# Performance work log

Measured on AMD Instinct MI355X. Metric: run time of the kernel, lower is better.

## Reference

```python
import jax, jax.numpy as jnp
import numpy as np

IN_F = 4096
OUT_F = 4096
NNZ = 167772  # int(IN_F*OUT_F*0.01)
B, S = 4, 2048
ALPHA = 1.0  # self.alpha (privacy enabled)


def setup_inputs() -> dict:
    key = jax.random.key(0)
    k1, k2, k3, k4, k5 = jax.random.split(key, 5)
    x = jax.random.normal(k1, (B, S, IN_F), dtype=jnp.float32)
    # quantized-then-dequantized base weights stored in fp16
    base_weights = (jax.random.normal(k2, (OUT_F, IN_F), dtype=jnp.float32) * 0.02).astype(jnp.float16)
    # sparse outlier residual in COO form (equivalent to the module's CSR buffers)
    ortho_rows = jax.random.randint(k3, (NNZ,), 0, OUT_F, dtype=jnp.int32)
    ortho_cols = jax.random.randint(k4, (NNZ,), 0, IN_F, dtype=jnp.int32)
    ortho_vals = (jax.random.normal(k5, (NNZ,), dtype=jnp.float32) * 1e-3).astype(jnp.float16)
    return {"x": x, "base_weights": base_weights, "ortho_vals": ortho_vals,
            "ortho_rows": ortho_rows, "ortho_cols": ortho_cols}


def reference(x, base_weights, ortho_vals, ortho_rows, ortho_cols):
    orig_shape = x.shape
    orig_dtype = x.dtype
    x_flat = x.reshape(-1, IN_F)                                   # [N, in]
    # Base stream: fp16 GEMM, accumulated to fp32 (matches torch.mm on fp16 then .to(f32))
    out_base = jnp.matmul(x_flat.astype(jnp.float16), base_weights.T).astype(jnp.float32)  # [N, out]
    # Ortho stream: sparse CSR residual, computed in fp32 (vals upcast like the module)
    # Scatter the nnz outliers into a dense [out, in] matrix once, then a single GEMM
    # (same math as torch.sparse.mm over the CSR tensor, without per-chunk loops).
    w_ortho = jnp.zeros((OUT_F, IN_F), jnp.float32).at[ortho_rows, ortho_cols].add(
        ortho_vals.astype(jnp.float32))
    out_ortho = jnp.matmul(x_flat.astype(jnp.float32), w_ortho.T)  # [N, out]
    out_flat = out_base + ALPHA * out_ortho
    return out_flat.reshape(orig_shape[:-1] + (OUT_F,)).astype(orig_dtype)
```

## Files before the change

kernel.cpp:

```cpp
#include <hip/hip_runtime.h>
#include <stdint.h>

#define IN_F 4096
#define OUT_F 4096
#define NTOK 8192
#define NNZ_CNT 167772

typedef __attribute__((ext_vector_type(4))) float f32x4;
typedef __attribute__((ext_vector_type(8))) __bf16 bf16x8;
typedef __attribute__((ext_vector_type(8))) unsigned short u16x8;

__device__ __forceinline__ unsigned short f2bf(float f) {
  union { float f; unsigned int i; } u; u.f = f;
  unsigned int i = u.i;
  unsigned int r = (i + 0x7FFFu + ((i >> 16) & 1u)) >> 16;
  return (unsigned short)r;
}
__device__ __forceinline__ float bf2f(unsigned short h) {
  union { unsigned int i; float f; } u; u.i = ((unsigned int)h) << 16;
  return u.f;
}
__device__ __forceinline__ float sanitize(float f, float lim) {
  if (f >= -lim && f <= lim) return f;
  if (f > lim) return lim;
  if (f < -lim) return -lim;
  return 0.f;
}

__device__ __forceinline__ bool detect_isf32(const unsigned short* w, int tid, int* sh_cnt) {
  if (tid == 0) *sh_cnt = 0;
  __syncthreads();
  int local = 0;
  if (tid < 256) {
    for (int j = 0; j < 16; ++j) {
      unsigned short u = w[tid * 16 + j];
      int e = (u >> 7) & 0xFF;
      if (u != 0 && e >= 107 && e <= 126) local++;
    }
  }
  atomicAdd(sh_cnt, local);
  __syncthreads();
  return *sh_cnt < 3481;
}

__global__ void prep_kernel(const float4* __restrict__ x, u16x8* __restrict__ xb, int n8x,
                            const void* __restrict__ bw, u16x8* __restrict__ wc, int n8w) {
  __shared__ int sh_cnt;
  const bool isf32 = detect_isf32((const unsigned short*)bw, threadIdx.x, &sh_cnt);
  const int stride = gridDim.x * blockDim.x;
  const int i0 = blockIdx.x * blockDim.x + threadIdx.x;
  for (int i = i0; i < n8x; i += stride) {
    float4 v0 = x[i * 2], v1 = x[i * 2 + 1];
    u16x8 o;
    o[0] = f2bf(sanitize(v0.x, 64.f)); o[1] = f2bf(sanitize(v0.y, 64.f));
    o[2] = f2bf(sanitize(v0.z, 64.f)); o[3] = f2bf(sanitize(v0.w, 64.f));
    o[4] = f2bf(sanitize(v1.x, 64.f)); o[5] = f2bf(sanitize(v1.y, 64.f));
    o[6] = f2bf(sanitize(v1.z, 64.f)); o[7] = f2bf(sanitize(v1.w, 64.f));
    xb[i] = o;
  }
  for (int i = i0; i < n8w; i += stride) {
    u16x8 o;
    if (isf32) {
      const float4* s = (const float4*)bw + i * 2;
      float4 v0 = s[0], v1 = s[1];
      o[0] = f2bf(sanitize(v0.x, 1.f)); o[1] = f2bf(sanitize(v0.y, 1.f));
      o[2] = f2bf(sanitize(v0.z, 1.f)); o[3] = f2bf(sanitize(v0.w, 1.f));
      o[4] = f2bf(sanitize(v1.x, 1.f)); o[5] = f2bf(sanitize(v1.y, 1.f));
      o[6] = f2bf(sanitize(v1.z, 1.f)); o[7] = f2bf(sanitize(v1.w, 1.f));
    } else {
      u16x8 v = ((const u16x8*)bw)[i];
#pragma unroll
      for (int j = 0; j < 8; ++j) o[j] = f2bf(sanitize(bf2f(v[j]), 1.f));
    }
    wc[i] = o;
  }
}

__global__ void scatter_kernel(const void* __restrict__ vals,
                               const int* __restrict__ rows,
                               const int* __restrict__ cols,
                               unsigned short* __restrict__ W,
                               const void* __restrict__ bw_probe) {
  __shared__ int sh_cnt;
  const bool isf32 = detect_isf32((const unsigned short*)bw_probe, threadIdx.x, &sh_cnt);
  int i = blockIdx.x * blockDim.x + threadIdx.x;
  if (i >= NNZ_CNT) return;
  int r = rows[i], c = cols[i];
  if ((unsigned)r >= OUT_F || (unsigned)c >= IN_F) return;
  float v = isf32 ? ((const float*)vals)[i] : bf2f(((const unsigned short*)vals)[i]);
  v = sanitize(v, 1.f);
  unsigned int* addr = (unsigned int*)(W + (size_t)r * IN_F + (c & ~1));
  bool hi = (c & 1);
  unsigned int old = *addr, assumed;
  do {
    assumed = old;
    unsigned short h = hi ? (unsigned short)(assumed >> 16) : (unsigned short)(assumed & 0xFFFFu);
    unsigned short nh = f2bf(bf2f(h) + v);
    unsigned int nw = hi ? ((assumed & 0x0000FFFFu) | ((unsigned int)nh << 16))
                         : ((assumed & 0xFFFF0000u) | (unsigned int)nh);
    old = atomicCAS(addr, assumed, nw);
  } while (old != assumed);
}

#define GLOAD16(g, l)                                                                  \
  __builtin_amdgcn_global_load_lds((const __attribute__((address_space(1))) void*)(g), \
                                   (__attribute__((address_space(3))) void*)(l), 16, 0, 0)

__global__ __launch_bounds__(512, 2) void gemm256_kernel(
    const unsigned short* __restrict__ Abf,
    const unsigned short* __restrict__ Bw,
    float* __restrict__ C) {
  __shared__ __align__(16) char lds[131072];
  const int t = threadIdx.x;
  const int l = t & 63;
  const int wv = t >> 6;
  const int wm = wv >> 2;
  const int wn = wv & 3;
  const int l15 = l & 15;

  const int swz = (blockIdx.x & 7) * 64 + (blockIdx.x >> 3);
  const int bm = (swz >> 4) * 256;
  const int bn = (swz & 15) * 256;

  const int srow = t >> 2;
  const int sunit = (t & 3) ^ ((t >> 3) & 3);
  const unsigned short* aS0 = Abf + (size_t)(bm + srow) * IN_F + sunit * 8;
  const unsigned short* aS1 = aS0 + (size_t)128 * IN_F;
  const unsigned short* bS0 = Bw + (size_t)(bn + srow) * IN_F + sunit * 8;
  const unsigned short* bS1 = bS0 + (size_t)128 * IN_F;
  char* dstA = (char*)lds + wv * 1024;
  char* dstB = (char*)lds + 32768 + wv * 1024;

  const int u = (l >> 4) ^ ((l15 >> 1) & 3);
  const int iA = (wm * 128 + l15) * 4 + u;
  const int iB = 2048 + (wn * 64 + l15) * 4 + u;
  const bf16x8* smp = (const bf16x8*)lds;

  f32x4 acc[8][4] = {};

  GLOAD16(aS0 + 0, dstA + 0);          GLOAD16(aS1 + 0, dstA + 8192);
  GLOAD16(bS0 + 0, dstB + 0);          GLOAD16(bS1 + 0, dstB + 8192);
  GLOAD16(aS0 + 32, dstA + 16384);     GLOAD16(aS1 + 32, dstA + 16384 + 8192);
  GLOAD16(bS0 + 32, dstB + 16384);     GLOAD16(bS1 + 32, dstB + 16384 + 8192);
  GLOAD16(aS0 + 64, dstA + 65536);     GLOAD16(aS1 + 64, dstA + 65536 + 8192);
  GLOAD16(bS0 + 64, dstB + 65536);     GLOAD16(bS1 + 64, dstB + 65536 + 8192);

  for (int kt = 0; kt < 64; ++kt) {
    const int c = kt & 1;
    const int cU = c << 12;
    const int s1 = ((kt + 1 < 64) ? (kt + 1) : 63) * 64 + 32;
    const int s2 = ((kt + 2 < 64) ? (kt + 2) : 63) * 64;
    const int d1 = (c ^ 1) * 65536 + 16384;
    const int d2 = c * 65536;
    bf16x8 av[4], bv[4], av1[8], bv1[4];

    asm volatile("s_waitcnt vmcnt(4)" ::: "memory");
    asm volatile("s_barrier" ::: "memory");

#pragma unroll
    for (int mi = 0; mi < 4; ++mi) av[mi] = smp[cU + iA + mi * 64];
#pragma unroll
    for (int ni = 0; ni < 4; ++ni) bv[ni] = smp[cU + iB + ni * 64];
    GLOAD16(aS0 + s1, dstA + d1);
    GLOAD16(aS1 + s1, dstA + d1 + 8192);
    __builtin_amdgcn_s_setprio(1);
#pragma unroll
    for (int mi = 0; mi < 4; ++mi)
#pragma unroll
      for (int ni = 0; ni < 4; ++ni)
        acc[mi][ni] = __builtin_amdgcn_mfma_f32_16x16x32_bf16(av[mi], bv[ni], acc[mi][ni], 0, 0, 0);
    __builtin_amdgcn_s_setprio(0);

#pragma unroll
    for (int mi = 0; mi < 4; ++mi) av[mi] = smp[cU + iA + (mi + 4) * 64];
    GLOAD16(bS0 + s1, dstB + d1);
    GLOAD16(bS1 + s1, dstB + d1 + 8192);
    __builtin_amdgcn_s_setprio(1);
#pragma unroll
    for (int mi = 0; mi < 4; ++mi)
#pragma unroll
      for (int ni = 0; ni < 4; ++ni)
        acc[mi + 4][ni] = __builtin_amdgcn_mfma_f32_16x16x32_bf16(av[mi], bv[ni], acc[mi + 4][ni], 0, 0, 0);
    __builtin_amdgcn_s_setprio(0);

#pragma unroll
    for (int mi = 0; mi < 8; ++mi) av1[mi] = smp[cU + 1024 + iA + mi * 64];
#pragma unroll
    for (int ni = 0; ni < 4; ++ni) bv1[ni] = smp[cU + 1024 + iB + ni * 64];

    asm volatile("s_barrier" ::: "memory");
    asm volatile("s_waitcnt lgkmcnt(0)" ::: "memory");

    GLOAD16(aS0 + s2, dstA + d2);
    GLOAD16(aS1 + s2, dstA + d2 + 8192);
    __builtin_amdgcn_s_setprio(1);
#pragma unroll
    for (int mi = 0; mi < 4; ++mi)
#pragma unroll
      for (int ni = 0; ni < 4; ++ni)
        acc[mi][ni] = __builtin_amdgcn_mfma_f32_16x16x32_bf16(av1[mi], bv1[ni], acc[mi][ni], 0, 0, 0);
    __builtin_amdgcn_s_setprio(0);

    GLOAD16(bS0 + s2, dstB + d2);
    GLOAD16(bS1 + s2, dstB + d2 + 8192);
    __builtin_amdgcn_s_setprio(1);
#pragma unroll
    for (int mi = 0; mi < 4; ++mi)
#pragma unroll
      for (int ni = 0; ni < 4; ++ni)
        acc[mi + 4][ni] = __builtin_amdgcn_mfma_f32_16x16x32_bf16(av1[mi + 4], bv1[ni], acc[mi + 4][ni], 0, 0, 0);
    __builtin_amdgcn_s_setprio(0);
  }

#pragma unroll
  for (int mi = 0; mi < 8; ++mi) {
#pragma unroll
    for (int ni = 0; ni < 4; ++ni) {
      int row0 = bm + wm * 128 + mi * 16 + ((l >> 4) << 2);
      int col = bn + wn * 64 + ni * 16 + l15;
#pragma unroll
      for (int r = 0; r < 4; ++r)
        C[(size_t)(row0 + r) * OUT_F + col] = acc[mi][ni][r];
    }
  }
}

__global__ __launch_bounds__(256, 3) void gemm_kernel(
    const float* __restrict__ Af, const unsigned short* __restrict__ Bw, float* __restrict__ C) {
  __shared__ bf16x8 smem[2048];
  const int tid = threadIdx.x;
  const int lane = tid & 63;
  const int wv = tid >> 6;
  const int bm = blockIdx.x * 128;
  const int bn = blockIdx.y * 128;
  const int srow = wv * 8 + (lane >> 3);
  const int scol = (lane & 7) * 8;
  const int wr = wv >> 1, wc = wv & 1;
  f32x4 acc[4][4] = {};
  const float* afp[4];
  const unsigned short* bptr[4];
#pragma unroll
  for (int q = 0; q < 4; ++q) {
    afp[q] = Af + (size_t)(bm + q * 32 + srow) * IN_F + scol;
    bptr[q] = Bw + (size_t)(bn + q * 32 + srow) * IN_F + scol;
  }
  char* smbase = (char*)smem;
  for (int k0 = 0; k0 < IN_F; k0 += 64) {
    __syncthreads();
#pragma unroll
    for (int q = 0; q < 4; ++q)
      GLOAD16(bptr[q] + k0, smbase + 16384 + q * 4096 + wv * 1024);
#pragma unroll
    for (int q = 0; q < 4; ++q) {
      const float* s = afp[q] + k0;
      float4 v0 = ((const float4*)s)[0];
      float4 v1 = ((const float4*)s)[1];
      u16x8 p;
      p[0] = f2bf(sanitize(v0.x, 64.f)); p[1] = f2bf(sanitize(v0.y, 64.f));
      p[2] = f2bf(sanitize(v0.z, 64.f)); p[3] = f2bf(sanitize(v0.w, 64.f));
      p[4] = f2bf(sanitize(v1.x, 64.f)); p[5] = f2bf(sanitize(v1.y, 64.f));
      p[6] = f2bf(sanitize(v1.z, 64.f)); p[7] = f2bf(sanitize(v1.w, 64.f));
      ((u16x8*)smem)[q * 256 + wv * 64 + lane] = p;
    }
    __syncthreads();
#pragma unroll
    for (int kk = 0; kk < 2; ++kk) {
      bf16x8 av[4], bv[4];
#pragma unroll
      for (int m = 0; m < 4; ++m)
        av[m] = smem[(wr * 64 + m * 16 + (lane & 15)) * 8 + kk * 4 + (lane >> 4)];
#pragma unroll
      for (int n = 0; n < 4; ++n)
        bv[n] = smem[1024 + (wc * 64 + n * 16 + (lane & 15)) * 8 + kk * 4 + (lane >> 4)];
#pragma unroll
      for (int m = 0; m < 4; ++m)
#pragma unroll
        for (int n = 0; n < 4; ++n)
          acc[m][n] = __builtin_amdgcn_mfma_f32_16x16x32_bf16(av[m], bv[n], acc[m][n], 0, 0, 0);
    }
  }
#pragma unroll
  for (int m = 0; m < 4; ++m)
#pragma unroll
    for (int n = 0; n < 4; ++n) {
      int row0 = bm + wr * 64 + m * 16 + ((lane >> 4) << 2);
      int col = bn + wc * 64 + n * 16 + (lane & 15);
#pragma unroll
      for (int r = 0; r < 4; ++r)
        C[(size_t)(row0 + r) * OUT_F + col] = acc[m][n][r];
    }
}

__global__ void naive_gemm_kernel(const float* __restrict__ x, const void* __restrict__ W,
                                  float* __restrict__ out) {
  __shared__ int sh_cnt;
  const bool isf32 = detect_isf32((const unsigned short*)W, threadIdx.x, &sh_cnt);
  int o = blockIdx.x * 256 + threadIdx.x;
  int t = blockIdx.y;
  const float* xr = x + (size_t)t * IN_F;
  float acc = 0.f;
  if (isf32) {
    const float* wr = (const float*)W + (size_t)o * IN_F;
    for (int k = 0; k < IN_F; ++k) acc += bf2f(f2bf(xr[k])) * bf2f(f2bf(sanitize(wr[k], 1.f)));
  } else {
    const unsigned short* wr = (const unsigned short*)W + (size_t)o * IN_F;
    for (int k = 0; k < IN_F; ++k) acc += bf2f(f2bf(xr[k])) * sanitize(bf2f(wr[k]), 1.f);
  }
  out[(size_t)t * OUT_F + o] = acc;
}
__global__ void naive_sparse_kernel(const float* __restrict__ x, const void* __restrict__ vals,
                                    const int* __restrict__ rows, const int* __restrict__ cols,
                                    float* __restrict__ out, const void* __restrict__ bw_probe) {
  __shared__ int sh_cnt;
  const bool isf32 = detect_isf32((const unsigned short*)bw_probe, threadIdx.x, &sh_cnt);
  int t = blockIdx.x * 256 + threadIdx.x;
  if (t >= NTOK) return;
  const float* xr = x + (size_t)t * IN_F;
  float* orow = out + (size_t)t * OUT_F;
  for (int i = 0; i < NNZ_CNT; ++i) {
    int r = rows[i], c = cols[i];
    if ((unsigned)r >= OUT_F || (unsigned)c >= IN_F) continue;
    float v = isf32 ? ((const float*)vals)[i] : bf2f(((const unsigned short*)vals)[i]);
    orow[r] += sanitize(v, 1.f) * xr[c];
  }
}

extern "C" void kernel_launch(void* const* d_in, const int* in_sizes, int n_in,
                              void* d_out, int out_size, void* d_ws, size_t ws_size,
                              hipStream_t stream) {
  (void)out_size;
  const int NX = NTOK * IN_F, NW = OUT_F * IN_F;
  int ix = -1, ib = -1, qs[3], nq = 0;
  for (int i = 0; i < n_in; ++i) {
    if (in_sizes[i] == NX) ix = i;
    else if (in_sizes[i] == NW) ib = i;
    else if (in_sizes[i] == NNZ_CNT && nq < 3) qs[nq++] = i;
  }
  if (ix < 0 || ib < 0 || nq < 3) { ix = 0; ib = 1; qs[0] = 2; qs[1] = 3; qs[2] = 4; }
  const float* x = (const float*)d_in[ix];
  const void* bw = d_in[ib];
  const int* rows = (const int*)d_in[qs[1]];
  const void* vals;
  const int* cols;
  if (ix < ib) { vals = d_in[qs[0]]; cols = (const int*)d_in[qs[2]]; }
  else         { vals = d_in[qs[2]]; cols = (const int*)d_in[qs[0]]; }
  float* out = (float*)d_out;

  const size_t w_bytes = (size_t)OUT_F * IN_F * 2;
  const size_t xb_bytes = (size_t)NTOK * IN_F * 2;

  if (ws_size < w_bytes + 64) {
    hipLaunchKernelGGL(naive_gemm_kernel, dim3(OUT_F / 256, NTOK), dim3(256), 0, stream,
                       x, bw, out);
    hipLaunchKernelGGL(naive_sparse_kernel, dim3((NTOK + 255) / 256), dim3(256), 0, stream,
                       x, vals, rows, cols, out, bw);
    return;
  }

  unsigned short* wcmb = (unsigned short*)d_ws;
  const bool big = ws_size >= w_bytes + xb_bytes;
  unsigned short* xb = (unsigned short*)((char*)d_ws + w_bytes);

  hipLaunchKernelGGL(prep_kernel, dim3(2048), dim3(256), 0, stream,
                     (const float4*)x, (u16x8*)xb, big ? (NX / 8) : 0,
                     bw, (u16x8*)wcmb, NW / 8);
  hipLaunchKernelGGL(scatter_kernel, dim3((NNZ_CNT + 255) / 256), dim3(256), 0, stream,
                     vals, rows, cols, wcmb, bw);

  if (big) {
    hipLaunchKernelGGL(gemm256_kernel, dim3((NTOK / 256) * (OUT_F / 256)), dim3(512), 0, stream,
                       xb, wcmb, out);
  } else {
    hipLaunchKernelGGL(gemm_kernel, dim3(NTOK / 128, OUT_F / 128), dim3(256), 0, stream,
                       x, wcmb, out);
  }
}
```

Measured before the change: 306.4 us.

## Shrink GEMM tile to 256x128 with triple-buffered K=32 stages

Reshapes the main bf16 GEMM block tile from 256x256 to 256x128. The 8 waves now form a 4x2 grid, each holding 64x64 accumulators instead of 128x64. The K loop changes from a double-buffered 64-wide step with split halves to a three-stage ring of 32-wide K slices, and LDS drops from 128KB to 72KB. The intent is to raise occupancy (launch bounds 4) and block count, for better latency hiding and load balance. The cost is less operand reuse per tile, more global/L2 traffic for the activations, and a barrier every 32 K instead of every 64.

```diff
diff --git a/kernel.cpp b/kernel.cpp
--- a/kernel.cpp
+++ b/kernel.cpp
@@ -106,63 +106,61 @@
   __builtin_amdgcn_global_load_lds((const __attribute__((address_space(1))) void*)(g), \
                                    (__attribute__((address_space(3))) void*)(l), 16, 0, 0)
 
-__global__ __launch_bounds__(512, 2) void gemm256_kernel(
+__global__ __launch_bounds__(512, 4) void gemm256_kernel(
     const unsigned short* __restrict__ Abf,
     const unsigned short* __restrict__ Bw,
     float* __restrict__ C) {
-  __shared__ __align__(16) char lds[131072];
+  __shared__ __align__(16) char lds[73728];
   const int t = threadIdx.x;
   const int l = t & 63;
   const int wv = t >> 6;
-  const int wm = wv >> 2;
-  const int wn = wv & 3;
+  const int wm = wv >> 1;
+  const int wn = wv & 1;
   const int l15 = l & 15;
 
-  const int swz = (blockIdx.x & 7) * 64 + (blockIdx.x >> 3);
-  const int bm = (swz >> 4) * 256;
-  const int bn = (swz & 15) * 256;
+  const int swz = (blockIdx.x & 7) * 128 + (blockIdx.x >> 3);
+  const int bm = (swz >> 5) * 256;
+  const int bn = (swz & 31) * 128;
 
   const int srow = t >> 2;
   const int sunit = (t & 3) ^ ((t >> 3) & 3);
   const unsigned short* aS0 = Abf + (size_t)(bm + srow) * IN_F + sunit * 8;
   const unsigned short* aS1 = aS0 + (size_t)128 * IN_F;
   const unsigned short* bS0 = Bw + (size_t)(bn + srow) * IN_F + sunit * 8;
-  const unsigned short* bS1 = bS0 + (size_t)128 * IN_F;
   char* dstA = (char*)lds + wv * 1024;
-  char* dstB = (char*)lds + 32768 + wv * 1024;
+  char* dstB = (char*)lds + 16384 + wv * 1024;
 
   const int u = (l >> 4) ^ ((l15 >> 1) & 3);
-  const int iA = (wm * 128 + l15) * 4 + u;
-  const int iB = 2048 + (wn * 64 + l15) * 4 + u;
+  const int iA = (wm * 64 + l15) * 4 + u;
+  const int iB = 1024 + (wn * 64 + l15) * 4 + u;
   const bf16x8* smp = (const bf16x8*)lds;
 
-  f32x4 acc[8][4] = {};
-
-  GLOAD16(aS0 + 0, dstA + 0);          GLOAD16(aS1 + 0, dstA + 8192);
-  GLOAD16(bS0 + 0, dstB + 0);          GLOAD16(bS1 + 0, dstB + 8192);
-  GLOAD16(aS0 + 32, dstA + 16384);     GLOAD16(aS1 + 32, dstA + 16384 + 8192);
-  GLOAD16(bS0 + 32, dstB + 16384);     GLOAD16(bS1 + 32, dstB + 16384 + 8192);
-  GLOAD16(aS0 + 64, dstA + 65536);     GLOAD16(aS1 + 64, dstA + 65536 + 8192);
-  GLOAD16(bS0 + 64, dstB + 65536);     GLOAD16(bS1 + 64, dstB + 65536 + 8192);
-
-  for (int kt = 0; kt < 64; ++kt) {
-    const int c = kt & 1;
-    const int cU = c << 12;
-    const int s1 = ((kt + 1 < 64) ? (kt + 1) : 63) * 64 + 32;
-    const int s2 = ((kt + 2 < 64) ? (kt + 2) : 63) * 64;
-    const int d1 = (c ^ 1) * 65536 + 16384;
-    const int d2 = c * 65536;
-    bf16x8 av[4], bv[4], av1[8], bv1[4];
-
-    asm volatile("s_waitcnt vmcnt(4)" ::: "memory");
+  f32x4 acc[4][4] = {};
+
+  GLOAD16(aS0 + 0, dstA + 0);
+  GLOAD16(aS1 + 0, dstA + 8192);
+  GLOAD16(bS0 + 0, dstB + 0);
+  GLOAD16(aS0 + 32, dstA + 24576);
+  GLOAD16(aS1 + 32, dstA + 24576 + 8192);
+  GLOAD16(bS0 + 32, dstB + 24576);
+
+  int c = 0;
+  for (int kt = 0; kt < 128; ++kt) {
+    const int c2 = (c >= 1) ? c - 1 : 2;
+    const int cU = c * 1536;
+    const int dA2 = c2 * 24576;
+    const int s2 = ((kt + 2 < 128) ? (kt + 2) : 127) * 32;
+    bf16x8 av[4], bv[4];
+
+    asm volatile("s_waitcnt vmcnt(3)" ::: "memory");
     asm volatile("s_barrier" ::: "memory");
-
 #pragma unroll
     for (int mi = 0; mi < 4; ++mi) av[mi] = smp[cU + iA + mi * 64];
+    GLOAD16(aS0 + s2, dstA + dA2);
+    GLOAD16(aS1 + s2, dstA + dA2 + 8192);
 #pragma unroll
     for (int ni = 0; ni < 4; ++ni) bv[ni] = smp[cU + iB + ni * 64];
-    GLOAD16(aS0 + s1, dstA + d1);
-    GLOAD16(aS1 + s1, dstA + d1 + 8192);
+    GLOAD16(bS0 + s2, dstB + dA2);
     __builtin_amdgcn_s_setprio(1);
 #pragma unroll
     for (int mi = 0; mi < 4; ++mi)
@@ -171,52 +169,14 @@
         acc[mi][ni] = __builtin_amdgcn_mfma_f32_16x16x32_bf16(av[mi], bv[ni], acc[mi][ni], 0, 0, 0);
     __builtin_amdgcn_s_setprio(0);
 
-#pragma unroll
-    for (int mi = 0; mi < 4; ++mi) av[mi] = smp[cU + iA + (mi + 4) * 64];
-    GLOAD16(bS0 + s1, dstB + d1);
-    GLOAD16(bS1 + s1, dstB + d1 + 8192);
-    __builtin_amdgcn_s_setprio(1);
-#pragma unroll
-    for (int mi = 0; mi < 4; ++mi)
-#pragma unroll
-      for (int ni = 0; ni < 4; ++ni)
-        acc[mi + 4][ni] = __builtin_amdgcn_mfma_f32_16x16x32_bf16(av[mi], bv[ni], acc[mi + 4][ni], 0, 0, 0);
-    __builtin_amdgcn_s_setprio(0);
-
-#pragma unroll
-    for (int mi = 0; mi < 8; ++mi) av1[mi] = smp[cU + 1024 + iA + mi * 64];
-#pragma unroll
-    for (int ni = 0; ni < 4; ++ni) bv1[ni] = smp[cU + 1024 + iB + ni * 64];
-
-    asm volatile("s_barrier" ::: "memory");
-    asm volatile("s_waitcnt lgkmcnt(0)" ::: "memory");
-
-    GLOAD16(aS0 + s2, dstA + d2);
-    GLOAD16(aS1 + s2, dstA + d2 + 8192);
-    __builtin_amdgcn_s_setprio(1);
-#pragma unroll
-    for (int mi = 0; mi < 4; ++mi)
-#pragma unroll
-      for (int ni = 0; ni < 4; ++ni)
-        acc[mi][ni] = __builtin_amdgcn_mfma_f32_16x16x32_bf16(av1[mi], bv1[ni], acc[mi][ni], 0, 0, 0);
-    __builtin_amdgcn_s_setprio(0);
-
-    GLOAD16(bS0 + s2, dstB + d2);
-    GLOAD16(bS1 + s2, dstB + d2 + 8192);
-    __builtin_amdgcn_s_setprio(1);
-#pragma unroll
-    for (int mi = 0; mi < 4; ++mi)
-#pragma unroll
-      for (int ni = 0; ni < 4; ++ni)
-        acc[mi + 4][ni] = __builtin_amdgcn_mfma_f32_16x16x32_bf16(av1[mi + 4], bv1[ni], acc[mi + 4][ni], 0, 0, 0);
-    __builtin_amdgcn_s_setprio(0);
-  }
-
-#pragma unroll
-  for (int mi = 0; mi < 8; ++mi) {
+    c = (c < 2) ? c + 1 : 0;
+  }
+
+#pragma unroll
+  for (int mi = 0; mi < 4; ++mi) {
 #pragma unroll
     for (int ni = 0; ni < 4; ++ni) {
-      int row0 = bm + wm * 128 + mi * 16 + ((l >> 4) << 2);
+      int row0 = bm + wm * 64 + mi * 16 + ((l >> 4) << 2);
       int col = bn + wn * 64 + ni * 16 + l15;
 #pragma unroll
       for (int r = 0; r < 4; ++r)
@@ -368,7 +328,7 @@
                      vals, rows, cols, wcmb, bw);
 
   if (big) {
-    hipLaunchKernelGGL(gemm256_kernel, dim3((NTOK / 256) * (OUT_F / 256)), dim3(512), 0, stream,
+    hipLaunchKernelGGL(gemm256_kernel, dim3((NTOK / 256) * (OUT_F / 128)), dim3(512), 0, stream,
                        xb, wcmb, out);
   } else {
     hipLaunchKernelGGL(gemm_kernel, dim3(NTOK / 128, OUT_F / 128), dim3(256), 0, stream,
```

Measured after the change: 348.5 us. +13.7%, slower.
